# Optimization experiments

Hardware: AMD Instinct MI355X
Metric: run time of the kernel (lower is better)

## Reference

```python
import jax, jax.numpy as jnp
import numpy as np
import math

D_MODEL = 768
N_HEADS = 12
D_HEAD = D_MODEL // N_HEADS


def setup_inputs() -> dict:
    key = jax.random.key(0)
    ks = jax.random.split(key, 5)
    x = jax.random.normal(ks[0], (2, 4096, D_MODEL), dtype=jnp.float32)
    s = 1.0 / math.sqrt(D_MODEL)
    W_qkv = jax.random.normal(ks[1], (D_MODEL, 3 * D_MODEL), dtype=jnp.float32) * s
    b_qkv = jnp.zeros((3 * D_MODEL,), dtype=jnp.float32)
    W_out = jax.random.normal(ks[2], (D_MODEL, D_MODEL), dtype=jnp.float32) * s
    b_out = jnp.zeros((D_MODEL,), dtype=jnp.float32)
    return {"x": x, "W_qkv": W_qkv, "b_qkv": b_qkv, "W_out": W_out, "b_out": b_out}


def reference(x, W_qkv, b_qkv, W_out, b_out):
    B, T, C = x.shape
    H, Dh = N_HEADS, D_HEAD
    qkv = x @ W_qkv + b_qkv                      # [B,T,3C]
    q, k, v = jnp.split(qkv, 3, axis=-1)
    q = q.reshape(B, T, H, Dh).transpose(0, 2, 1, 3)  # [B,H,T,Dh]
    k = k.reshape(B, T, H, Dh).transpose(0, 2, 1, 3)
    v = v.reshape(B, T, H, Dh).transpose(0, 2, 1, 3)
    att = jnp.einsum('bhqd,bhkd->bhqk', q, k) * (1.0 / math.sqrt(Dh))
    causal = jnp.tril(jnp.ones((T, T), dtype=bool))
    att = jnp.where(causal, att, -jnp.inf)
    att = jax.nn.softmax(att, axis=-1)
    out = jnp.einsum('bhqk,bhkd->bhqd', att, v)  # [B,H,T,Dh]
    out = out.transpose(0, 2, 1, 3).reshape(B, T, C)
    return out @ W_out + b_out
```

## Files before the change

kernel.cpp:

```cpp
#include <hip/hip_runtime.h>
#include <hip/hip_bf16.h>
#include <cstdint>

#define NH 12
#define DH 64
#define TSEQ 4096
#define BATCH 2
#define CDIM 768
#define MROWS (BATCH*TSEQ)

typedef __bf16 bf16x8 __attribute__((ext_vector_type(8)));
typedef __bf16 bf16x4 __attribute__((ext_vector_type(4)));
typedef bf16x8 bf16x8_a __attribute__((may_alias));
typedef bf16x4 bf16x4_a __attribute__((may_alias));
typedef float f32x4 __attribute__((ext_vector_type(4)));

__device__ __forceinline__ uint16_t f2bu(float f) {
  uint32_t u = __float_as_uint(f);
  u += 0x7fffu + ((u >> 16) & 1u);
  return (uint16_t)(u >> 16);
}

__device__ __forceinline__ float bu2f(uint16_t x) {
  return __uint_as_float(((uint32_t)x) << 16);
}

__device__ __forceinline__ void gload_lds16(const void* g, void* l) {
  __builtin_amdgcn_global_load_lds(
      (const __attribute__((address_space(1))) void*)g,
      (__attribute__((address_space(3))) void*)l, 16, 0, 0);
}

__global__ void cast_f32_bf16(const float* __restrict__ in, uint16_t* __restrict__ out, int n4) {
  int i = blockIdx.x * blockDim.x + threadIdx.x;
  int stride = gridDim.x * blockDim.x;
  for (; i < n4; i += stride) {
    float4 v = ((const float4*)in)[i];
    ushort4 o;
    o.x = f2bu(v.x); o.y = f2bu(v.y); o.z = f2bu(v.z); o.w = f2bu(v.w);
    ((ushort4*)out)[i] = o;
  }
}

__global__ void transpose_cast(const float* __restrict__ w, uint16_t* __restrict__ wt, int K, int N) {
  __shared__ float tile[32][33];
  int kb = blockIdx.x * 32, nb = blockIdx.y * 32;
  int tx = threadIdx.x & 31, ty = threadIdx.x >> 5;
  #pragma unroll
  for (int r = ty; r < 32; r += 8) tile[r][tx] = w[(size_t)(kb + r) * N + nb + tx];
  __syncthreads();
  #pragma unroll
  for (int r = ty; r < 32; r += 8) wt[(size_t)(nb + r) * K + kb + tx] = f2bu(tile[tx][r]);
}

template <int MODE>
__global__ __launch_bounds__(256) void gemm_bt(
    const uint16_t* __restrict__ A, const uint16_t* __restrict__ Bt,
    const float* __restrict__ bias,
    uint16_t* __restrict__ q, uint16_t* __restrict__ k, uint16_t* __restrict__ v,
    float* __restrict__ outf, int N, int K) {
  __shared__ uint16_t As[128 * 32];
  __shared__ uint16_t Bs[128 * 32];
  int tid = threadIdx.x;
  int w = tid >> 6, l = tid & 63;
  int lg = l >> 4, lr = l & 15;
  int mb = blockIdx.x * 128, nb = blockIdx.y * 128;
  int wr = (w >> 1) * 64, wc = (w & 1) * 64;
  f32x4 acc[4][4] = {};
  int srow = tid >> 2, scol = (tid & 3) * 8;
  const uint16_t* Ag = A + (size_t)(mb + srow) * K + scol;
  const uint16_t* Bg = Bt + (size_t)(nb + srow) * K + scol;
  char* AsB = (char*)As + (size_t)w * 1024;
  char* BsB = (char*)Bs + (size_t)w * 1024;
  size_t rowskip = (size_t)64 * K;
  for (int kb = 0; kb < K; kb += 32) {
    __syncthreads();
    gload_lds16(Ag + kb, AsB);
    gload_lds16(Ag + kb + rowskip, AsB + 4096);
    gload_lds16(Bg + kb, BsB);
    gload_lds16(Bg + kb + rowskip, BsB + 4096);
    __syncthreads();
    bf16x8 af[4], bfr[4];
    #pragma unroll
    for (int i = 0; i < 4; ++i)
      af[i] = *(const bf16x8_a*)(const void*)(As + (wr + i * 16 + lr) * 32 + lg * 8);
    #pragma unroll
    for (int i = 0; i < 4; ++i)
      bfr[i] = *(const bf16x8_a*)(const void*)(Bs + (wc + i * 16 + lr) * 32 + lg * 8);
    #pragma unroll
    for (int mi = 0; mi < 4; ++mi)
      #pragma unroll
      for (int ni = 0; ni < 4; ++ni)
        acc[mi][ni] = __builtin_amdgcn_mfma_f32_16x16x32_bf16(af[mi], bfr[ni], acc[mi][ni], 0, 0, 0);
  }
  #pragma unroll
  for (int mi = 0; mi < 4; ++mi) {
    #pragma unroll
    for (int ni = 0; ni < 4; ++ni) {
      if (MODE == 0) {
        int gm0 = mb + wr + mi * 16 + lg * 4;
        int gn = nb + wc + ni * 16 + lr;
        int which = gn / CDIM;
        int cc = gn - which * CDIM;
        int hh = cc >> 6, d = cc & 63;
        float bs = bias[gn];
        if (which == 2) {
          int b0 = gm0 >> 12, t0 = gm0 & 4095;
          ushort4 pk;
          pk.x = f2bu(acc[mi][ni][0] + bs);
          pk.y = f2bu(acc[mi][ni][1] + bs);
          pk.z = f2bu(acc[mi][ni][2] + bs);
          pk.w = f2bu(acc[mi][ni][3] + bs);
          *(ushort4*)&v[(((size_t)(b0 * NH + hh)) * DH + d) * TSEQ + t0] = pk;
        } else {
          uint16_t* dst = which ? k : q;
          float sc = which ? 1.0f : 0.1803368801111204f;
          #pragma unroll
          for (int j = 0; j < 4; ++j) {
            int gm = gm0 + j;
            int bb = gm >> 12, t = gm & 4095;
            float val = (acc[mi][ni][j] + bs) * sc;
            dst[(((size_t)(bb * NH + hh)) * TSEQ + t) * DH + d] = f2bu(val);
          }
        }
      } else {
        #pragma unroll
        for (int j = 0; j < 4; ++j) {
          int gm = mb + wr + mi * 16 + lg * 4 + j;
          int gn = nb + wc + ni * 16 + lr;
          outf[(size_t)gm * N + gn] = acc[mi][ni][j] + bias[gn];
        }
      }
    }
  }
}

__global__ __launch_bounds__(256) void attn_part(
    const uint16_t* __restrict__ Q, const uint16_t* __restrict__ K,
    const uint16_t* __restrict__ Vt, uint16_t* __restrict__ O,
    uint16_t* __restrict__ Pbuf, float* __restrict__ Plsum) {
  int gid = blockIdx.x;
  int widx = gid / 24, bh = gid - widx * 24;
  int qt, t0, t1, chunk;
  bool direct;
  if (widx < 32) {
    qt = 31 - (widx >> 1); chunk = widx & 1; direct = false;
    t0 = chunk ? (qt + 1) : 0;
    t1 = chunk ? (2 * qt + 1) : qt;
  } else {
    qt = 47 - widx; chunk = 0; direct = true;
    t0 = 0; t1 = 2 * qt + 1;
  }
  int b = bh / NH, hd = bh - b * NH;
  size_t base = (size_t)bh * TSEQ * DH;
  int tid = threadIdx.x, w = tid >> 6, lane = tid & 63;
  int lg = lane >> 4, lr = lane & 15;
  __shared__ __align__(16) uint16_t Ks[2][64 * 64];
  __shared__ __align__(16) uint16_t Vs[2][64 * 64];
  __shared__ uint16_t Ps[4][16 * 64];
  char* pw = (char*)Ps[w];
  int srow = tid >> 3;
  int schunk = (tid & 7) ^ (srow & 7);
  const uint16_t* Kg0 = K + base + (size_t)srow * DH + schunk * 8;
  const uint16_t* Vg0 = Vt + base + (size_t)srow * TSEQ + schunk * 8;
  int swzA = (lg ^ (lr & 7)) << 4;
  int swzB = swzA ^ 64;

  int qb = qt * 128;
  int qgA = qb + w * 16 + lr;
  int qgB = qgA + 64;
  bf16x8 qA0 = *(const bf16x8_a*)(const void*)(Q + base + (size_t)qgA * DH + lg * 8);
  bf16x8 qA1 = *(const bf16x8_a*)(const void*)(Q + base + (size_t)qgA * DH + 32 + lg * 8);
  bf16x8 qB0 = *(const bf16x8_a*)(const void*)(Q + base + (size_t)qgB * DH + lg * 8);
  bf16x8 qB1 = *(const bf16x8_a*)(const void*)(Q + base + (size_t)qgB * DH + 32 + lg * 8);
  f32x4 oA[4] = {}, oB[4] = {};
  float lA = 0.f, lB = 0.f;
  int lg4 = lg * 4;
  int pofs = (lg & 1) * 8;

#define STAGE(bufi, tv) do { \
    char* kd_ = (char*)Ks[bufi] + w * 1024; \
    char* vd_ = (char*)Vs[bufi] + w * 1024; \
    const uint16_t* kg_ = Kg0 + (size_t)(tv) * (64 * DH); \
    const uint16_t* vg_ = Vg0 + (size_t)(tv) * 64; \
    gload_lds16(kg_,           kd_); \
    gload_lds16(kg_ + 32 * DH, kd_ + 4096); \
    gload_lds16(vg_,                     vd_); \
    gload_lds16(vg_ + (size_t)32 * TSEQ, vd_ + 4096); \
  } while (0)

  STAGE(0, t0);
  __syncthreads();
  int cur = 0;
  for (int t = t0; t <= t1; ++t) {
    if (t + 1 <= t1) STAGE(cur ^ 1, t + 1);
    const uint16_t* Kc = Ks[cur];
    const uint16_t* Vc = Vs[cur];
    bool doA = (t <= 2 * qt);
    int kb0 = t * 64;
    f32x4 sA[4], sB[4];
    __builtin_amdgcn_s_setprio(1);
    #pragma unroll
    for (int ni = 0; ni < 4; ++ni) {
      const char* kbp = (const char*)Kc + (ni * 16 + lr) * 128;
      bf16x8 kf0 = *(const bf16x8_a*)(kbp + swzA);
      bf16x8 kf1 = *(const bf16x8_a*)(kbp + swzB);
      f32x4 s = {};
      s = __builtin_amdgcn_mfma_f32_16x16x32_bf16(kf0, qB0, s, 0, 0, 0);
      s = __builtin_amdgcn_mfma_f32_16x16x32_bf16(kf1, qB1, s, 0, 0, 0);
      sB[ni] = s;
      if (doA) {
        f32x4 sa = {};
        sa = __builtin_amdgcn_mfma_f32_16x16x32_bf16(kf0, qA0, sa, 0, 0, 0);
        sa = __builtin_amdgcn_mfma_f32_16x16x32_bf16(kf1, qA1, sa, 0, 0, 0);
        sA[ni] = sa;
      }
    }
    __builtin_amdgcn_s_setprio(0);
    bf16x8 pfA0, pfA1;
    if (doA) {
      if (t == 2 * qt) {
        int thr = qgA - kb0 - lg4;
        #pragma unroll
        for (int ni = 0; ni < 4; ++ni)
          #pragma unroll
          for (int j = 0; j < 4; ++j)
            sA[ni][j] = (16 * ni + j <= thr) ? sA[ni][j] : -1e30f;
      }
      #pragma unroll
      for (int ni = 0; ni < 4; ++ni) {
        float p0 = __builtin_amdgcn_exp2f(sA[ni][0]);
        float p1 = __builtin_amdgcn_exp2f(sA[ni][1]);
        float p2 = __builtin_amdgcn_exp2f(sA[ni][2]);
        float p3 = __builtin_amdgcn_exp2f(sA[ni][3]);
        lA += (p0 + p1) + (p2 + p3);
        bf16x4 pk;
        pk[0] = (__bf16)p0; pk[1] = (__bf16)p1; pk[2] = (__bf16)p2; pk[3] = (__bf16)p3;
        int chunkc = (2 * ni + (lg >> 1)) ^ (lr & 7);
        *(bf16x4_a*)(pw + lr * 128 + chunkc * 16 + pofs) = pk;
      }
      pfA0 = *(const bf16x8_a*)(pw + lr * 128 + swzA);
      pfA1 = *(const bf16x8_a*)(pw + lr * 128 + swzB);
    }
    {
      if (t == 2 * qt + 1) {
        int thr = qgB - kb0 - lg4;
        #pragma unroll
        for (int ni = 0; ni < 4; ++ni)
          #pragma unroll
          for (int j = 0; j < 4; ++j)
            sB[ni][j] = (16 * ni + j <= thr) ? sB[ni][j] : -1e30f;
      }
      #pragma unroll
      for (int ni = 0; ni < 4; ++ni) {
        float p0 = __builtin_amdgcn_exp2f(sB[ni][0]);
        float p1 = __builtin_amdgcn_exp2f(sB[ni][1]);
        float p2 = __builtin_amdgcn_exp2f(sB[ni][2]);
        float p3 = __builtin_amdgcn_exp2f(sB[ni][3]);
        lB += (p0 + p1) + (p2 + p3);
        bf16x4 pk;
        pk[0] = (__bf16)p0; pk[1] = (__bf16)p1; pk[2] = (__bf16)p2; pk[3] = (__bf16)p3;
        int chunkc = (2 * ni + (lg >> 1)) ^ (lr & 7);
        *(bf16x4_a*)(pw + lr * 128 + chunkc * 16 + pofs) = pk;
      }
    }
    bf16x8 pfB0 = *(const bf16x8_a*)(pw + lr * 128 + swzA);
    bf16x8 pfB1 = *(const bf16x8_a*)(pw + lr * 128 + swzB);
    __builtin_amdgcn_s_setprio(1);
    #pragma unroll
    for (int nd = 0; nd < 4; ++nd) {
      const char* vb = (const char*)Vc + (nd * 16 + lr) * 128;
      bf16x8 vf0 = *(const bf16x8_a*)(vb + swzA);
      bf16x8 vf1 = *(const bf16x8_a*)(vb + swzB);
      oB[nd] = __builtin_amdgcn_mfma_f32_16x16x32_bf16(pfB0, vf0, oB[nd], 0, 0, 0);
      oB[nd] = __builtin_amdgcn_mfma_f32_16x16x32_bf16(pfB1, vf1, oB[nd], 0, 0, 0);
      if (doA) {
        oA[nd] = __builtin_amdgcn_mfma_f32_16x16x32_bf16(pfA0, vf0, oA[nd], 0, 0, 0);
        oA[nd] = __builtin_amdgcn_mfma_f32_16x16x32_bf16(pfA1, vf1, oA[nd], 0, 0, 0);
      }
    }
    __builtin_amdgcn_s_setprio(0);
    __syncthreads();
    cur ^= 1;
  }
#undef STAGE

  lA += __shfl_xor(lA, 16, 64); lA += __shfl_xor(lA, 32, 64);
  lB += __shfl_xor(lB, 16, 64); lB += __shfl_xor(lB, 32, 64);
  if (direct) {
    float riA = 1.0f / lA, riB = 1.0f / lB;
    #pragma unroll
    for (int j = 0; j < 4; ++j) {
      float rvA = __shfl(riA, (lane & 48) | (lg4 + j), 64);
      float rvB = __shfl(riB, (lane & 48) | (lg4 + j), 64);
      int tA = qb + w * 16 + lg4 + j;
      size_t pA = (size_t)(b * TSEQ + tA) * CDIM + hd * DH + lr;
      size_t pB = pA + (size_t)64 * CDIM;
      #pragma unroll
      for (int nd = 0; nd < 4; ++nd) {
        O[pA + nd * 16] = f2bu(oA[nd][j] * rvA);
        O[pB + nd * 16] = f2bu(oB[nd][j] * rvB);
      }
    }
  } else {
    int pidx = (bh << 4) + (qt - 16);
    uint16_t* Pb = Pbuf + ((size_t)pidx * 2 + chunk) * 8192;
    float* Pl = Plsum + ((size_t)pidx * 2 + chunk) * 128;
    #pragma unroll
    for (int j = 0; j < 4; ++j) {
      int qlA = w * 16 + lg4 + j;
      #pragma unroll
      for (int nd = 0; nd < 4; ++nd) {
        Pb[qlA * 64 + nd * 16 + lr] = f2bu(oA[nd][j]);
        Pb[(64 + qlA) * 64 + nd * 16 + lr] = f2bu(oB[nd][j]);
      }
    }
    if (lane < 16) {
      Pl[w * 16 + lane] = lA;
      Pl[64 + w * 16 + lane] = lB;
    }
  }
}

__global__ __launch_bounds__(256) void attn_reduce(
    const uint16_t* __restrict__ Pbuf, const float* __restrict__ Plsum,
    uint16_t* __restrict__ O) {
  int pidx = blockIdx.x;
  int bh = pidx >> 4, qrel = pidx & 15;
  int qt = 16 + qrel;
  int b = bh / NH, hd = bh - b * NH;
  int d = threadIdx.x & 63, qo = threadIdx.x >> 6;
  const uint16_t* p0 = Pbuf + (size_t)pidx * 2 * 8192;
  const uint16_t* p1 = p0 + 8192;
  const float* l0 = Plsum + (size_t)pidx * 2 * 128;
  const float* l1 = l0 + 128;
  #pragma unroll 4
  for (int q = qo; q < 128; q += 4) {
    float li = 1.0f / (l0[q] + l1[q]);
    float s = bu2f(p0[q * 64 + d]) + bu2f(p1[q * 64 + d]);
    int t = qt * 128 + q;
    O[(size_t)(b * TSEQ + t) * CDIM + hd * DH + d] = f2bu(s * li);
  }
}

extern "C" void kernel_launch(void* const* d_in, const int* in_sizes, int n_in,
                              void* d_out, int out_size, void* d_ws, size_t ws_size,
                              hipStream_t stream) {
  const float* x    = (const float*)d_in[0];
  const float* Wqkv = (const float*)d_in[1];
  const float* bqkv = (const float*)d_in[2];
  const float* Wout = (const float*)d_in[3];
  const float* bout = (const float*)d_in[4];
  float* out = (float*)d_out;
  char* ws = (char*)d_ws;

  uint16_t* Xb    = (uint16_t*)(ws + 0);
  uint16_t* Wqkvt = (uint16_t*)(ws + 12582912);
  uint16_t* Woutt = (uint16_t*)(ws + 16121856);
  uint16_t* Qb    = (uint16_t*)(ws + 17301504);
  uint16_t* Kb    = (uint16_t*)(ws + 29884416);
  uint16_t* Vtb   = (uint16_t*)(ws + 42467328);
  uint16_t* Ob    = (uint16_t*)(ws + 55050240);
  uint16_t* Pbuf  = Xb;
  float*    Plsum = (float*)Wqkvt;

  cast_f32_bf16<<<2048, 256, 0, stream>>>(x, Xb, (MROWS * CDIM) / 4);
  transpose_cast<<<dim3(24, 72), 256, 0, stream>>>(Wqkv, Wqkvt, 768, 2304);
  transpose_cast<<<dim3(24, 24), 256, 0, stream>>>(Wout, Woutt, 768, 768);
  gemm_bt<0><<<dim3(64, 18), 256, 0, stream>>>(Xb, Wqkvt, bqkv, Qb, Kb, Vtb, nullptr, 2304, 768);
  attn_part<<<1152, 256, 0, stream>>>(Qb, Kb, Vtb, Ob, Pbuf, Plsum);
  attn_reduce<<<384, 256, 0, stream>>>(Pbuf, Plsum, Ob);
  gemm_bt<1><<<dim3(64, 6), 256, 0, stream>>>(Ob, Woutt, bout, nullptr, nullptr, nullptr, out, 768, 768);
}
```

Measured before the change: 194.9 us.

## Single-buffer attention K/V staging and retile out-projection GEMM to 128x64

The attention kernel drops its double-buffered K/V shared-memory staging in favour of a single buffer loaded synchronously each iteration. This cuts LDS use, likely to allow more resident blocks, at the cost of losing load/compute overlap. The output projection GEMM becomes a separate kernel with 128x64 tiles and twice as many blocks, to improve CU utilisation for the small N=768 GEMM.

```diff
diff --git a/kernel.cpp b/kernel.cpp
--- a/kernel.cpp
+++ b/kernel.cpp
@@ -53,12 +53,11 @@
   for (int r = ty; r < 32; r += 8) wt[(size_t)(nb + r) * K + kb + tx] = f2bu(tile[tx][r]);
 }
 
-template <int MODE>
-__global__ __launch_bounds__(256) void gemm_bt(
+__global__ __launch_bounds__(256) void gemm_qkv(
     const uint16_t* __restrict__ A, const uint16_t* __restrict__ Bt,
     const float* __restrict__ bias,
     uint16_t* __restrict__ q, uint16_t* __restrict__ k, uint16_t* __restrict__ v,
-    float* __restrict__ outf, int N, int K) {
+    int N, int K) {
   __shared__ uint16_t As[128 * 32];
   __shared__ uint16_t Bs[128 * 32];
   int tid = threadIdx.x;
@@ -97,39 +96,80 @@
   for (int mi = 0; mi < 4; ++mi) {
     #pragma unroll
     for (int ni = 0; ni < 4; ++ni) {
-      if (MODE == 0) {
-        int gm0 = mb + wr + mi * 16 + lg * 4;
-        int gn = nb + wc + ni * 16 + lr;
-        int which = gn / CDIM;
-        int cc = gn - which * CDIM;
-        int hh = cc >> 6, d = cc & 63;
-        float bs = bias[gn];
-        if (which == 2) {
-          int b0 = gm0 >> 12, t0 = gm0 & 4095;
-          ushort4 pk;
-          pk.x = f2bu(acc[mi][ni][0] + bs);
-          pk.y = f2bu(acc[mi][ni][1] + bs);
-          pk.z = f2bu(acc[mi][ni][2] + bs);
-          pk.w = f2bu(acc[mi][ni][3] + bs);
-          *(ushort4*)&v[(((size_t)(b0 * NH + hh)) * DH + d) * TSEQ + t0] = pk;
-        } else {
-          uint16_t* dst = which ? k : q;
-          float sc = which ? 1.0f : 0.1803368801111204f;
-          #pragma unroll
-          for (int j = 0; j < 4; ++j) {
-            int gm = gm0 + j;
-            int bb = gm >> 12, t = gm & 4095;
-            float val = (acc[mi][ni][j] + bs) * sc;
-            dst[(((size_t)(bb * NH + hh)) * TSEQ + t) * DH + d] = f2bu(val);
-          }
-        }
+      int gm0 = mb + wr + mi * 16 + lg * 4;
+      int gn = nb + wc + ni * 16 + lr;
+      int which = gn / CDIM;
+      int cc = gn - which * CDIM;
+      int hh = cc >> 6, d = cc & 63;
+      float bs = bias[gn];
+      if (which == 2) {
+        int b0 = gm0 >> 12, t0 = gm0 & 4095;
+        ushort4 pk;
+        pk.x = f2bu(acc[mi][ni][0] + bs);
+        pk.y = f2bu(acc[mi][ni][1] + bs);
+        pk.z = f2bu(acc[mi][ni][2] + bs);
+        pk.w = f2bu(acc[mi][ni][3] + bs);
+        *(ushort4*)&v[(((size_t)(b0 * NH + hh)) * DH + d) * TSEQ + t0] = pk;
       } else {
+        uint16_t* dst = which ? k : q;
+        float sc = which ? 1.0f : 0.1803368801111204f;
         #pragma unroll
         for (int j = 0; j < 4; ++j) {
-          int gm = mb + wr + mi * 16 + lg * 4 + j;
-          int gn = nb + wc + ni * 16 + lr;
-          outf[(size_t)gm * N + gn] = acc[mi][ni][j] + bias[gn];
+          int gm = gm0 + j;
+          int bb = gm >> 12, t = gm & 4095;
+          float val = (acc[mi][ni][j] + bs) * sc;
+          dst[(((size_t)(bb * NH + hh)) * TSEQ + t) * DH + d] = f2bu(val);
         }
+      }
+    }
+  }
+}
+
+__global__ __launch_bounds__(256) void gemm_out(
+    const uint16_t* __restrict__ A, const uint16_t* __restrict__ Bt,
+    const float* __restrict__ bias, float* __restrict__ outf, int N, int K) {
+  __shared__ uint16_t As[128 * 32];
+  __shared__ uint16_t Bs[64 * 32];
+  int tid = threadIdx.x;
+  int w = tid >> 6, l = tid & 63;
+  int lg = l >> 4, lr = l & 15;
+  int mb = blockIdx.x * 128, nb = blockIdx.y * 64;
+  int wr = w * 32;
+  f32x4 acc[2][4] = {};
+  int srow = tid >> 2, scol = (tid & 3) * 8;
+  const uint16_t* Ag = A + (size_t)(mb + srow) * K + scol;
+  const uint16_t* Bg = Bt + (size_t)(nb + srow) * K + scol;
+  char* AsB = (char*)As + (size_t)w * 1024;
+  char* BsB = (char*)Bs + (size_t)w * 1024;
+  size_t rowskip = (size_t)64 * K;
+  for (int kb = 0; kb < K; kb += 32) {
+    __syncthreads();
+    gload_lds16(Ag + kb, AsB);
+    gload_lds16(Ag + kb + rowskip, AsB + 4096);
+    gload_lds16(Bg + kb, BsB);
+    __syncthreads();
+    bf16x8 af[2], bfr[4];
+    #pragma unroll
+    for (int i = 0; i < 2; ++i)
+      af[i] = *(const bf16x8_a*)(const void*)(As + (wr + i * 16 + lr) * 32 + lg * 8);
+    #pragma unroll
+    for (int i = 0; i < 4; ++i)
+      bfr[i] = *(const bf16x8_a*)(const void*)(Bs + (i * 16 + lr) * 32 + lg * 8);
+    #pragma unroll
+    for (int mi = 0; mi < 2; ++mi)
+      #pragma unroll
+      for (int ni = 0; ni < 4; ++ni)
+        acc[mi][ni] = __builtin_amdgcn_mfma_f32_16x16x32_bf16(af[mi], bfr[ni], acc[mi][ni], 0, 0, 0);
+  }
+  #pragma unroll
+  for (int mi = 0; mi < 2; ++mi) {
+    #pragma unroll
+    for (int ni = 0; ni < 4; ++ni) {
+      #pragma unroll
+      for (int j = 0; j < 4; ++j) {
+        int gm = mb + wr + mi * 16 + lg * 4 + j;
+        int gn = nb + ni * 16 + lr;
+        outf[(size_t)gm * N + gn] = acc[mi][ni][j] + bias[gn];
       }
     }
   }
@@ -155,14 +195,16 @@
   size_t base = (size_t)bh * TSEQ * DH;
   int tid = threadIdx.x, w = tid >> 6, lane = tid & 63;
   int lg = lane >> 4, lr = lane & 15;
-  __shared__ __align__(16) uint16_t Ks[2][64 * 64];
-  __shared__ __align__(16) uint16_t Vs[2][64 * 64];
+  __shared__ __align__(16) uint16_t Ks[64 * 64];
+  __shared__ __align__(16) uint16_t Vs[64 * 64];
   __shared__ uint16_t Ps[4][16 * 64];
   char* pw = (char*)Ps[w];
   int srow = tid >> 3;
   int schunk = (tid & 7) ^ (srow & 7);
   const uint16_t* Kg0 = K + base + (size_t)srow * DH + schunk * 8;
   const uint16_t* Vg0 = Vt + base + (size_t)srow * TSEQ + schunk * 8;
+  char* KsB = (char*)Ks + w * 1024;
+  char* VsB = (char*)Vs + w * 1024;
   int swzA = (lg ^ (lr & 7)) << 4;
   int swzB = swzA ^ 64;
 
@@ -178,31 +220,24 @@
   int lg4 = lg * 4;
   int pofs = (lg & 1) * 8;
 
-#define STAGE(bufi, tv) do { \
-    char* kd_ = (char*)Ks[bufi] + w * 1024; \
-    char* vd_ = (char*)Vs[bufi] + w * 1024; \
-    const uint16_t* kg_ = Kg0 + (size_t)(tv) * (64 * DH); \
-    const uint16_t* vg_ = Vg0 + (size_t)(tv) * 64; \
-    gload_lds16(kg_,           kd_); \
-    gload_lds16(kg_ + 32 * DH, kd_ + 4096); \
-    gload_lds16(vg_,                     vd_); \
-    gload_lds16(vg_ + (size_t)32 * TSEQ, vd_ + 4096); \
-  } while (0)
-
-  STAGE(0, t0);
-  __syncthreads();
-  int cur = 0;
   for (int t = t0; t <= t1; ++t) {
-    if (t + 1 <= t1) STAGE(cur ^ 1, t + 1);
-    const uint16_t* Kc = Ks[cur];
-    const uint16_t* Vc = Vs[cur];
+    __syncthreads();
+    {
+      const uint16_t* kg_ = Kg0 + (size_t)t * (64 * DH);
+      const uint16_t* vg_ = Vg0 + (size_t)t * 64;
+      gload_lds16(kg_,           KsB);
+      gload_lds16(kg_ + 32 * DH, KsB + 4096);
+      gload_lds16(vg_,                     VsB);
+      gload_lds16(vg_ + (size_t)32 * TSEQ, VsB + 4096);
+    }
+    __syncthreads();
     bool doA = (t <= 2 * qt);
     int kb0 = t * 64;
     f32x4 sA[4], sB[4];
     __builtin_amdgcn_s_setprio(1);
     #pragma unroll
     for (int ni = 0; ni < 4; ++ni) {
-      const char* kbp = (const char*)Kc + (ni * 16 + lr) * 128;
+      const char* kbp = (const char*)Ks + (ni * 16 + lr) * 128;
       bf16x8 kf0 = *(const bf16x8_a*)(kbp + swzA);
       bf16x8 kf1 = *(const bf16x8_a*)(kbp + swzB);
       f32x4 s = {};
@@ -269,7 +304,7 @@
     __builtin_amdgcn_s_setprio(1);
     #pragma unroll
     for (int nd = 0; nd < 4; ++nd) {
-      const char* vb = (const char*)Vc + (nd * 16 + lr) * 128;
+      const char* vb = (const char*)Vs + (nd * 16 + lr) * 128;
       bf16x8 vf0 = *(const bf16x8_a*)(vb + swzA);
       bf16x8 vf1 = *(const bf16x8_a*)(vb + swzB);
       oB[nd] = __builtin_amdgcn_mfma_f32_16x16x32_bf16(pfB0, vf0, oB[nd], 0, 0, 0);
@@ -280,10 +315,7 @@
       }
     }
     __builtin_amdgcn_s_setprio(0);
-    __syncthreads();
-    cur ^= 1;
-  }
-#undef STAGE
+  }
 
   lA += __shfl_xor(lA, 16, 64); lA += __shfl_xor(lA, 32, 64);
   lB += __shfl_xor(lB, 16, 64); lB += __shfl_xor(lB, 32, 64);
@@ -367,8 +399,8 @@
   cast_f32_bf16<<<2048, 256, 0, stream>>>(x, Xb, (MROWS * CDIM) / 4);
   transpose_cast<<<dim3(24, 72), 256, 0, stream>>>(Wqkv, Wqkvt, 768, 2304);
   transpose_cast<<<dim3(24, 24), 256, 0, stream>>>(Wout, Woutt, 768, 768);
-  gemm_bt<0><<<dim3(64, 18), 256, 0, stream>>>(Xb, Wqkvt, bqkv, Qb, Kb, Vtb, nullptr, 2304, 768);
+  gemm_qkv<<<dim3(64, 18), 256, 0, stream>>>(Xb, Wqkvt, bqkv, Qb, Kb, Vtb, 2304, 768);
   attn_part<<<1152, 256, 0, stream>>>(Qb, Kb, Vtb, Ob, Pbuf, Plsum);
   attn_reduce<<<384, 256, 0, stream>>>(Pbuf, Plsum, Ob);
-  gemm_bt<1><<<dim3(64, 6), 256, 0, stream>>>(Ob, Woutt, bout, nullptr, nullptr, nullptr, out, 768, 768);
-}
+  gemm_out<<<dim3(64, 12), 256, 0, stream>>>(Ob, Woutt, bout, out, 768, 768);
+}
```

Result: no change. 191.5 us (-1.7%).
